# Kernel tuning notes

Measured on AMD Instinct MI355X. Metric: run time of the kernel, lower is better.

The kernel has to match this reference:

```python
import jax, jax.numpy as jnp
import numpy as np

NEG = -1e12


def setup_inputs() -> dict:
    key = jax.random.key(0)
    ks = jax.random.split(key, 6)
    B, S, D, H = 32, 2048, 1024, 1024  # batch, seq, dec/enc dim, hidden
    last_state = jax.random.normal(ks[0], (B, D), dtype=jnp.float32)
    enc_outputs = jax.random.normal(ks[1], (B, S, D), dtype=jnp.float32)
    attn_masks = jax.random.randint(ks[2], (B, S), 0, 2, dtype=jnp.int32)
    W = jax.random.normal(ks[3], (H, 2 * D), dtype=jnp.float32) * 0.02
    b = jax.random.normal(ks[4], (H,), dtype=jnp.float32) * 0.02
    V = jax.random.normal(ks[5], (H,), dtype=jnp.float32)
    return {"last_state": last_state, "enc_outputs": enc_outputs,
            "attn_masks": attn_masks, "W": W, "b": b, "V": V}


def reference(last_state, enc_outputs, attn_masks, W, b, V):
    # Split W to avoid materializing the [B,S,2D] concat:
    # concat([h, e]) @ W.T == h @ Wh.T + e @ We.T
    D = last_state.shape[-1]
    Wh, We = W[:, :D], W[:, D:]
    # hidden part: [B,H], broadcast over seq
    h_part = jnp.einsum('bd,hd->bh', last_state, Wh)  # [B,H]
    e_part = jnp.einsum('bsd,hd->bsh', enc_outputs, We)  # [B,S,H]
    sim = jnp.tanh(h_part[:, None, :] + e_part + b)  # [B,S,H]
    scores = jnp.einsum('bsh,h->bs', sim, V)  # [B,S]
    scores = jnp.where(attn_masks != 1, jnp.float32(NEG), scores)
    attn_weights = jax.nn.softmax(scores, axis=1)  # [B,S]
    context = jnp.einsum('bs,bsd->bd', attn_weights, enc_outputs)  # [B,D]
    return context, attn_weights, scores
```

## Files before the change

kernel.cpp:

```cpp
#include <hip/hip_runtime.h>
#include <math.h>
#include <stdint.h>

#define B_ 32
#define S_ 2048
#define D_ 1024
#define H_ 1024
#define NEGV -1000000000000.0f

typedef __attribute__((ext_vector_type(8))) short bf16x8;
typedef __attribute__((ext_vector_type(8))) _Float16 f16x8;
typedef __attribute__((ext_vector_type(4))) float f32x4;

static __device__ __forceinline__ unsigned short f2bf(float x) {
    union { float f; unsigned u; } v; v.f = x;
    unsigned r = v.u + 0x7FFF + ((v.u >> 16) & 1);
    return (unsigned short)(r >> 16);
}
static __device__ __forceinline__ float bf2f(unsigned short h) {
    union { float f; unsigned u; } v; v.u = ((unsigned)h) << 16; return v.f;
}
static __device__ __forceinline__ unsigned short f2h(float x) {
    _Float16 h = (_Float16)x; unsigned short u;
    __builtin_memcpy(&u, &h, 2); return u;
}
static __device__ __forceinline__ float h2f(unsigned short u) {
    _Float16 h; __builtin_memcpy(&h, &u, 2); return (float)h;
}
static __device__ __forceinline__ float tanh_fast(float x) {
    float e = __expf(2.f * x);
    return 1.f - 2.f / (e + 1.f);
}
static __device__ __forceinline__ void gl_lds16(unsigned short* lds, const unsigned short* g) {
    __builtin_amdgcn_global_load_lds(
        (const __attribute__((address_space(1))) unsigned int*)(const void*)g,
        (__attribute__((address_space(3))) unsigned int*)(void*)lds,
        16, 0, 0);
}

__global__ __launch_bounds__(256) void k_W_f16(const float* __restrict__ W,
                                               unsigned short* __restrict__ out) {
    int idx = blockIdx.x * 256 + threadIdx.x;
    int h = idx >> 7, kc = idx & 127;
    const float* src = W + (size_t)h * (2 * D_) + D_ + kc * 8;
    float4 a = *(const float4*)src;
    float4 c4 = *(const float4*)(src + 4);
    float v[8] = {a.x, a.y, a.z, a.w, c4.x, c4.y, c4.z, c4.w};
    unsigned short t[8];
#pragma unroll
    for (int j = 0; j < 8; ++j) t[j] = f2h(v[j]);
    uint4 w;
    w.x = t[0] | ((unsigned)t[1] << 16); w.y = t[2] | ((unsigned)t[3] << 16);
    w.z = t[4] | ((unsigned)t[5] << 16); w.w = t[6] | ((unsigned)t[7] << 16);
    int g = kc >> 4, cc = kc & 15;
    int dst = g * 128 + ((cc ^ (h & 15)) << 3);
    *(uint4*)(out + (size_t)h * D_ + dst) = w;
}

__global__ __launch_bounds__(256) void k_hpart(const float* __restrict__ ls,
                                               const float* __restrict__ W,
                                               float* __restrict__ hp) {
    int bh = blockIdx.x * 256 + threadIdx.x;
    int b = bh >> 10, h = bh & 1023;
    const float* lsr = ls + b * D_;
    const float* wr  = W + (size_t)h * (2 * D_);
    float acc = 0.f;
#pragma unroll 4
    for (int d = 0; d < D_; d += 4) {
        float4 a = *(const float4*)(lsr + d);
        float4 w = *(const float4*)(wr + d);
        acc += a.x * w.x + a.y * w.y + a.z * w.z + a.w * w.w;
    }
    hp[bh] = acc;
}

__global__ __launch_bounds__(512, 2) void k_scores_m128(
    const float* __restrict__ enc,
    const unsigned short* __restrict__ Wf16,
    const float* __restrict__ hp, const float* __restrict__ bias,
    const float* __restrict__ V, float* __restrict__ spart)
{
    extern __shared__ unsigned short smem[];
    unsigned short* smemA = smem;
    unsigned short* smemB = smem + 16384;

    const int tid  = threadIdx.x;
    const int lane = tid & 63, wid = tid >> 6;
    const int wm = wid >> 2, wn = wid & 3;
    const int l15 = lane & 15, lhi = lane >> 4;

    const int bid  = blockIdx.x;
    const int wgid = (bid & 7) * 256 + (bid >> 3);
    const int mt = wgid >> 2, nt = wgid & 3;
    const int m0 = mt * 128;
    const int nt256 = nt * 256;
    const int b = m0 >> 11;

    const size_t boff = (size_t)(nt256 + wid * 32 + (lane >> 4)) * D_ + (lane & 15) * 8;
    const int ldsb = wid * 4096;

    f32x4 acc[4][4];
#pragma unroll
    for (int i = 0; i < 4; ++i)
#pragma unroll
        for (int j = 0; j < 4; ++j)
            acc[i][j] = (f32x4){0.f, 0.f, 0.f, 0.f};

    const int swz = l15;

    float4 ar0[4], ar1[4];

#define LOAD_A(KOFS) do {                                                           \
    _Pragma("unroll")                                                               \
    for (int s_ = 0; s_ < 4; ++s_) {                                                \
        int p_ = tid + s_ * 512;                                                    \
        int row_ = p_ >> 4, pc_ = p_ & 15;                                          \
        const float* ap_ = enc + (size_t)(m0 + row_) * D_ + (KOFS) + pc_ * 8;       \
        ar0[s_] = *(const float4*)ap_;                                              \
        ar1[s_] = *(const float4*)(ap_ + 4);                                        \
    }                                                                               \
} while (0)
#define WRITE_A() do {                                                              \
    _Pragma("unroll")                                                               \
    for (int s_ = 0; s_ < 4; ++s_) {                                                \
        int p_ = tid + s_ * 512;                                                    \
        int row_ = p_ >> 4, pc_ = p_ & 15;                                          \
        float v_[8] = {ar0[s_].x, ar0[s_].y, ar0[s_].z, ar0[s_].w,                  \
                       ar1[s_].x, ar1[s_].y, ar1[s_].z, ar1[s_].w};                 \
        unsigned short t_[8];                                                       \
        _Pragma("unroll")                                                           \
        for (int j_ = 0; j_ < 8; ++j_) t_[j_] = f2h(v_[j_]);                        \
        uint4 w_;                                                                   \
        w_.x = t_[0] | ((unsigned)t_[1] << 16); w_.y = t_[2] | ((unsigned)t_[3] << 16); \
        w_.z = t_[4] | ((unsigned)t_[5] << 16); w_.w = t_[6] | ((unsigned)t_[7] << 16); \
        *(uint4*)&smemA[row_ * 128 + ((pc_ ^ (row_ & 15)) << 3)] = w_;              \
    }                                                                               \
} while (0)

#define STAGE_B(KOFS) do {                                                          \
    _Pragma("unroll")                                                               \
    for (int j_ = 0; j_ < 8; ++j_)                                                  \
        gl_lds16(&smemB[ldsb + j_ * 512], Wf16 + boff + (size_t)j_ * 4 * D_ + (KOFS)); \
} while (0)

#define LDA(AR, KS) do {                                                            \
    _Pragma("unroll")                                                               \
    for (int fi_ = 0; fi_ < 4; ++fi_) {                                             \
        int row_ = wm * 64 + fi_ * 16 + l15;                                        \
        int ch_  = ((KS) * 4 + lhi) ^ swz;                                          \
        AR[fi_] = *(const f16x8*)&smemA[row_ * 128 + ch_ * 8];                      \
    }                                                                               \
} while (0)
#define LDB(BR, KS) do {                                                            \
    _Pragma("unroll")                                                               \
    for (int fi_ = 0; fi_ < 4; ++fi_) {                                             \
        int row_ = wn * 64 + fi_ * 16 + l15;                                        \
        int ch_  = ((KS) * 4 + lhi) ^ swz;                                          \
        BR[fi_] = *(const f16x8*)&smemB[row_ * 128 + ch_ * 8];                      \
    }                                                                               \
} while (0)
#define MFMA16(AR, BR) do {                                                         \
    _Pragma("unroll")                                                               \
    for (int fi_ = 0; fi_ < 4; ++fi_)                                               \
    _Pragma("unroll")                                                               \
        for (int fj_ = 0; fj_ < 4; ++fj_)                                           \
            acc[fi_][fj_] = __builtin_amdgcn_mfma_f32_16x16x32_f16(                 \
                AR[fi_], BR[fj_], acc[fi_][fj_], 0, 0, 0);                          \
} while (0)

    LOAD_A(0);
    WRITE_A();
    STAGE_B(0);
    __syncthreads();

    f16x8 a[4], bk[4];
#pragma unroll 1
    for (int t = 0; t < 8; ++t) {
        const int kofs = (t + 1) * 128;

        if (t < 7) LOAD_A(kofs);

#pragma unroll
        for (int ks = 0; ks < 4; ++ks) {
            LDB(bk, ks);
            LDA(a, ks);
            MFMA16(a, bk);
        }

        __syncthreads();

        if (t < 7) {
            WRITE_A();
            STAGE_B(kofs);
        }

        __syncthreads();
    }

    float hb[4], vv[4];
#pragma unroll
    for (int fn = 0; fn < 4; ++fn) {
        int h = nt256 + wn * 64 + fn * 16 + l15;
        hb[fn] = hp[b * H_ + h] + bias[h];
        vv[fn] = V[h];
    }
    float* s_red = (float*)smem;
#pragma unroll
    for (int fm = 0; fm < 4; ++fm)
#pragma unroll
        for (int rg = 0; rg < 4; ++rg) {
            float rs = 0.f;
#pragma unroll
            for (int fn = 0; fn < 4; ++fn)
                rs += tanh_fast(acc[fm][fn][rg] + hb[fn]) * vv[fn];
            rs += __shfl_xor(rs, 1, 16);
            rs += __shfl_xor(rs, 2, 16);
            rs += __shfl_xor(rs, 4, 16);
            rs += __shfl_xor(rs, 8, 16);
            if (l15 == 0)
                s_red[wn * 128 + wm * 64 + fm * 16 + lhi * 4 + rg] = rs;
        }
    __syncthreads();
    if (tid < 128) {
        float v = s_red[tid] + s_red[128 + tid] + s_red[256 + tid] + s_red[384 + tid];
        spart[(size_t)nt * 65536 + m0 + tid] = v;
    }
#undef LOAD_A
#undef WRITE_A
#undef STAGE_B
#undef LDA
#undef LDB
#undef MFMA16
}

__global__ __launch_bounds__(256) void k_softmax_fold(const float* __restrict__ spart,
                                                      const int* __restrict__ mask,
                                                      float* __restrict__ scores_out,
                                                      float* __restrict__ weights) {
    __shared__ float red[8];
    int b = blockIdx.x, tid = threadIdx.x;
    float vals[8];
    float mx = -INFINITY;
#pragma unroll
    for (int i = 0; i < 8; ++i) {
        int m = b * S_ + tid + i * 256;
        float s = spart[m] + spart[65536 + m] + spart[131072 + m] + spart[196608 + m];
        s = (mask[m] == 1) ? s : NEGV;
        scores_out[m] = s;
        vals[i] = s;
        mx = fmaxf(mx, s);
    }
    for (int off = 32; off; off >>= 1) mx = fmaxf(mx, __shfl_xor(mx, off, 64));
    int wave = tid >> 6;
    if ((tid & 63) == 0) red[wave] = mx;
    __syncthreads();
    mx = fmaxf(fmaxf(red[0], red[1]), fmaxf(red[2], red[3]));
    float sum = 0.f;
#pragma unroll
    for (int i = 0; i < 8; ++i) {
        vals[i] = expf(vals[i] - mx);
        sum += vals[i];
    }
    for (int off = 32; off; off >>= 1) sum += __shfl_xor(sum, off, 64);
    if ((tid & 63) == 0) red[4 + wave] = sum;
    __syncthreads();
    sum = red[4] + red[5] + red[6] + red[7];
    float inv = 1.f / sum;
#pragma unroll
    for (int i = 0; i < 8; ++i)
        weights[b * S_ + tid + i * 256] = vals[i] * inv;
}

__global__ __launch_bounds__(256) void k_ctx_partial_f32(const float* __restrict__ weights,
                                                         const float* __restrict__ enc,
                                                         float* __restrict__ part) {
    int b = blockIdx.x >> 4;
    int chunk = blockIdx.x & 15;
    int tid = threadIdx.x;
    int d0 = tid * 4;
    float4 acc = {0.f, 0.f, 0.f, 0.f};
    int s0 = chunk * 128;
    const float* wrow = weights + b * S_;
    for (int s = s0; s < s0 + 128; ++s) {
        float w = wrow[s];
        if (w != 0.f) {
            float4 e = *(const float4*)(enc + (size_t)(b * S_ + s) * D_ + d0);
            acc.x += w * e.x; acc.y += w * e.y; acc.z += w * e.z; acc.w += w * e.w;
        }
    }
    *(float4*)(part + (size_t)blockIdx.x * D_ + d0) = acc;
}

__global__ __launch_bounds__(256) void k_ctx_reduce(const float* __restrict__ part,
                                                    float* __restrict__ ctx) {
    int bd = blockIdx.x * 256 + threadIdx.x;
    int b = bd >> 10, d = bd & 1023;
    float acc = 0.f;
#pragma unroll
    for (int c = 0; c < 16; ++c)
        acc += part[(size_t)(b * 16 + c) * D_ + d];
    ctx[bd] = acc;
}

__global__ __launch_bounds__(256) void k_splitW_lin(const float* __restrict__ W,
                                                    unsigned short* __restrict__ hi,
                                                    unsigned short* __restrict__ lo) {
    int idx = blockIdx.x * 256 + threadIdx.x;
    int h = idx >> 7, kc = idx & 127;
    const float* src = W + (size_t)h * (2 * D_) + D_ + kc * 8;
    float4 a = *(const float4*)src;
    float4 c = *(const float4*)(src + 4);
    float v[8] = {a.x, a.y, a.z, a.w, c.x, c.y, c.z, c.w};
    unsigned short th[8], tl[8];
#pragma unroll
    for (int j = 0; j < 8; ++j) {
        th[j] = f2bf(v[j]);
        tl[j] = f2bf(v[j] - bf2f(th[j]));
    }
    uint4 hw, lw;
    hw.x = th[0] | ((unsigned)th[1] << 16); hw.y = th[2] | ((unsigned)th[3] << 16);
    hw.z = th[4] | ((unsigned)th[5] << 16); hw.w = th[6] | ((unsigned)th[7] << 16);
    lw.x = tl[0] | ((unsigned)tl[1] << 16); lw.y = tl[2] | ((unsigned)tl[3] << 16);
    lw.z = tl[4] | ((unsigned)tl[5] << 16); lw.w = tl[6] | ((unsigned)tl[7] << 16);
    *(uint4*)(hi + (size_t)h * D_ + kc * 8) = hw;
    *(uint4*)(lo + (size_t)h * D_ + kc * 8) = lw;
}

__global__ __launch_bounds__(256, 2) void k_scores_mfma_fb(
    const float* __restrict__ enc,
    const unsigned short* __restrict__ Whi,
    const unsigned short* __restrict__ Wlo,
    const float* __restrict__ hp,
    const float* __restrict__ bias,
    const float* __restrict__ V,
    const int* __restrict__ mask,
    float* __restrict__ scores_out)
{
    __shared__ __align__(16) unsigned short smem[4 * 8192];
    unsigned short* sAhi = smem;
    unsigned short* sAlo = smem + 8192;
    unsigned short* sBhi = smem + 16384;
    unsigned short* sBlo = smem + 24576;

    const int tid  = threadIdx.x;
    const int lane = tid & 63, wid = tid >> 6;
    const int wr = wid >> 1, wc = wid & 1;
    const int l15 = lane & 15, lhi = lane >> 4;
    const int m0 = blockIdx.x * 128;
    const int b  = m0 >> 11;

    float rowsum[4][4] = {};
    float4 pa[8];
    uint4  pbh[4], pbl[4];

#define STAGE_LOAD(NB, KB) do {                                            \
    _Pragma("unroll")                                                      \
    for (int i_ = 0; i_ < 4; ++i_) {                                       \
        int c_ = tid + i_ * 256;                                           \
        int r_ = c_ >> 3, kc_ = c_ & 7;                                    \
        const float* ap_ = enc + (size_t)(m0 + r_) * D_ + (KB) * 64 + kc_ * 8; \
        pa[2 * i_]     = *(const float4*)ap_;                              \
        pa[2 * i_ + 1] = *(const float4*)(ap_ + 4);                        \
        size_t bo_ = (size_t)((NB) * 128 + r_) * D_ + (KB) * 64 + kc_ * 8; \
        pbh[i_] = *(const uint4*)(Whi + bo_);                              \
        pbl[i_] = *(const uint4*)(Wlo + bo_);                              \
    }                                                                      \
} while (0)

#define STAGE_WRITE() do {                                                 \
    _Pragma("unroll")                                                      \
    for (int i_ = 0; i_ < 4; ++i_) {                                       \
        int c_ = tid + i_ * 256;                                           \
        int sc_ = c_ ^ ((c_ >> 3) & 7);                                    \
        float vv_[8] = {pa[2*i_].x, pa[2*i_].y, pa[2*i_].z, pa[2*i_].w,    \
                        pa[2*i_+1].x, pa[2*i_+1].y, pa[2*i_+1].z, pa[2*i_+1].w}; \
        unsigned short th_[8], tl_[8];                                     \
        _Pragma("unroll")                                                  \
        for (int j_ = 0; j_ < 8; ++j_) {                                   \
            th_[j_] = f2bf(vv_[j_]);                                       \
            tl_[j_] = f2bf(vv_[j_] - bf2f(th_[j_]));                       \
        }                                                                  \
        uint4 hw_, lw_;                                                    \
        hw_.x = th_[0] | ((unsigned)th_[1] << 16); hw_.y = th_[2] | ((unsigned)th_[3] << 16); \
        hw_.z = th_[4] | ((unsigned)th_[5] << 16); hw_.w = th_[6] | ((unsigned)th_[7] << 16); \
        lw_.x = tl_[0] | ((unsigned)tl_[1] << 16); lw_.y = tl_[2] | ((unsigned)tl_[3] << 16); \
        lw_.z = tl_[4] | ((unsigned)tl_[5] << 16); lw_.w = tl_[6] | ((unsigned)tl_[7] << 16); \
        *(uint4*)&sAhi[sc_ * 8] = hw_;                                     \
        *(uint4*)&sAlo[sc_ * 8] = lw_;                                     \
        *(uint4*)&sBhi[sc_ * 8] = pbh[i_];                                 \
        *(uint4*)&sBlo[sc_ * 8] = pbl[i_];                                 \
    }                                                                      \
} while (0)

    STAGE_LOAD(0, 0);

    for (int nb = 0; nb < 8; ++nb) {
        f32x4 acc[4][4];
#pragma unroll
        for (int i = 0; i < 4; ++i)
#pragma unroll
            for (int j = 0; j < 4; ++j)
                acc[i][j] = (f32x4){0.f, 0.f, 0.f, 0.f};

        for (int kb = 0; kb < 16; ++kb) {
            __syncthreads();
            STAGE_WRITE();
            __syncthreads();
            int nkb = kb + 1, nnb = nb;
            if (nkb == 16) { nkb = 0; nnb = nb + 1; }
            if (nnb < 8) STAGE_LOAD(nnb, nkb);

#pragma unroll
            for (int ks = 0; ks < 2; ++ks) {
                bf16x8 bh[4], bl[4];
#pragma unroll
                for (int fn = 0; fn < 4; ++fn) {
                    int rB = wc * 64 + fn * 16 + l15;
                    int ch = (rB * 8 + ks * 4 + lhi) ^ (rB & 7);
                    bh[fn] = *(const bf16x8*)&sBhi[ch * 8];
                    bl[fn] = *(const bf16x8*)&sBlo[ch * 8];
                }
#pragma unroll
                for (int fm = 0; fm < 4; ++fm) {
                    int rA = wr * 64 + fm * 16 + l15;
                    int ch = (rA * 8 + ks * 4 + lhi) ^ (rA & 7);
                    bf16x8 ah = *(const bf16x8*)&sAhi[ch * 8];
                    bf16x8 al = *(const bf16x8*)&sAlo[ch * 8];
#pragma unroll
                    for (int fn = 0; fn < 4; ++fn) {
                        acc[fm][fn] = __builtin_amdgcn_mfma_f32_16x16x32_bf16(ah, bh[fn], acc[fm][fn], 0, 0, 0);
                        acc[fm][fn] = __builtin_amdgcn_mfma_f32_16x16x32_bf16(ah, bl[fn], acc[fm][fn], 0, 0, 0);
                        acc[fm][fn] = __builtin_amdgcn_mfma_f32_16x16x32_bf16(al, bh[fn], acc[fm][fn], 0, 0, 0);
                    }
                }
            }
        }

        int n0 = nb * 128;
#pragma unroll
        for (int fn = 0; fn < 4; ++fn) {
            int n = n0 + wc * 64 + fn * 16 + l15;
            float hbv = hp[b * H_ + n] + bias[n];
            float vvv = V[n];
#pragma unroll
            for (int fm = 0; fm < 4; ++fm) {
                f32x4 a = acc[fm][fn];
#pragma unroll
                for (int rg = 0; rg < 4; ++rg)
                    rowsum[fm][rg] += tanh_fast(a[rg] + hbv) * vvv;
            }
        }
    }

    __syncthreads();
    float* s_red = (float*)smem;
#pragma unroll
    for (int fm = 0; fm < 4; ++fm)
#pragma unroll
        for (int rg = 0; rg < 4; ++rg) {
            float v = rowsum[fm][rg];
            v += __shfl_xor(v, 1, 16);
            v += __shfl_xor(v, 2, 16);
            v += __shfl_xor(v, 4, 16);
            v += __shfl_xor(v, 8, 16);
            if (l15 == 0)
                s_red[wc * 128 + wr * 64 + fm * 16 + lhi * 4 + rg] = v;
        }
    __syncthreads();
    if (tid < 128) {
        int m = m0 + tid;
        float sc = s_red[tid] + s_red[128 + tid];
        scores_out[m] = (mask[m] == 1) ? sc : NEGV;
    }
#undef STAGE_LOAD
#undef STAGE_WRITE
}

__global__ __launch_bounds__(256) void k_softmax(const float* __restrict__ scores,
                                                 float* __restrict__ weights) {
    __shared__ float red[8];
    int b = blockIdx.x;
    int tid = threadIdx.x;
    const float* srow = scores + b * S_;
    float vals[8];
    float mx = -INFINITY;
#pragma unroll
    for (int i = 0; i < 8; ++i) {
        vals[i] = srow[tid + i * 256];
        mx = fmaxf(mx, vals[i]);
    }
    for (int off = 32; off; off >>= 1) mx = fmaxf(mx, __shfl_xor(mx, off, 64));
    int wave = tid >> 6;
    if ((tid & 63) == 0) red[wave] = mx;
    __syncthreads();
    mx = fmaxf(fmaxf(red[0], red[1]), fmaxf(red[2], red[3]));
    float sum = 0.f;
#pragma unroll
    for (int i = 0; i < 8; ++i) {
        vals[i] = expf(vals[i] - mx);
        sum += vals[i];
    }
    for (int off = 32; off; off >>= 1) sum += __shfl_xor(sum, off, 64);
    if ((tid & 63) == 0) red[4 + wave] = sum;
    __syncthreads();
    sum = red[4] + red[5] + red[6] + red[7];
    float inv = 1.f / sum;
#pragma unroll
    for (int i = 0; i < 8; ++i)
        weights[b * S_ + tid + i * 256] = vals[i] * inv;
}

extern "C" void kernel_launch(void* const* d_in, const int* in_sizes, int n_in,
                              void* d_out, int out_size, void* d_ws, size_t ws_size,
                              hipStream_t stream) {
    const float* ls   = (const float*)d_in[0];
    const float* enc  = (const float*)d_in[1];
    const int*   mask = (const int*)d_in[2];
    const float* W    = (const float*)d_in[3];
    const float* bias = (const float*)d_in[4];
    const float* V    = (const float*)d_in[5];

    float* out     = (float*)d_out;
    float* ctx     = out;
    float* weights = out + 32768;
    float* scores  = out + 98304;

    const size_t need = 2097152ull + 131072ull + 1048576ull + 2097152ull;

    if (ws_size >= need) {
        unsigned short* Wf16 = (unsigned short*)d_ws;
        float* hp    = (float*)(Wf16 + 1048576);
        float* spart = hp + 32768;
        float* part  = spart + 262144;

        hipFuncSetAttribute((const void*)k_scores_m128,
                            hipFuncAttributeMaxDynamicSharedMemorySize, 98304);

        k_W_f16<<<512, 256, 0, stream>>>(W, Wf16);
        k_hpart<<<128, 256, 0, stream>>>(ls, W, hp);
        k_scores_m128<<<2048, 512, 98304, stream>>>(enc, Wf16, hp, bias, V, spart);
        k_softmax_fold<<<32, 256, 0, stream>>>(spart, mask, scores, weights);
        k_ctx_partial_f32<<<512, 256, 0, stream>>>(weights, enc, part);
        k_ctx_reduce<<<128, 256, 0, stream>>>(part, ctx);
    } else {
        unsigned short* Whi = (unsigned short*)d_ws;
        unsigned short* Wlo = Whi + 1048576;
        float* hp   = (float*)(Wlo + 1048576);
        float* part = hp + 32768;

        k_splitW_lin<<<512, 256, 0, stream>>>(W, Whi, Wlo);
        k_hpart<<<128, 256, 0, stream>>>(ls, W, hp);
        k_scores_mfma_fb<<<512, 256, 0, stream>>>(enc, Whi, Wlo, hp, bias, V, mask, scores);
        k_softmax<<<32, 256, 0, stream>>>(scores, weights);
        k_ctx_partial_f32<<<512, 256, 0, stream>>>(weights, enc, part);
        k_ctx_reduce<<<128, 256, 0, stream>>>(part, ctx);
    }
}
```

Baseline: 288.1 us.

## Halve K-tile and drop register prefetch to raise scores GEMM occupancy

The scores GEMM kernel now uses a K-tile of 64 instead of 128, halving LDS per block to 48KB, and raises launch bounds to 4 blocks per CU. The register-staged software prefetch of the A tile is removed: each iteration loads and converts A and stages B, syncs, then computes. The W fp16 layout and swizzle are changed to match the 64-wide tile. Latency hiding now depends on more resident waves instead of explicit overlap, at the cost of twice as many barriers per K sweep and a tighter register budget.

```diff
diff --git a/kernel.cpp b/kernel.cpp
--- a/kernel.cpp
+++ b/kernel.cpp
@@ -52,8 +52,8 @@
     uint4 w;
     w.x = t[0] | ((unsigned)t[1] << 16); w.y = t[2] | ((unsigned)t[3] << 16);
     w.z = t[4] | ((unsigned)t[5] << 16); w.w = t[6] | ((unsigned)t[7] << 16);
-    int g = kc >> 4, cc = kc & 15;
-    int dst = g * 128 + ((cc ^ (h & 15)) << 3);
+    int g = kc >> 3, cc = kc & 7;
+    int dst = g * 64 + ((cc ^ (h & 7)) << 3);
     *(uint4*)(out + (size_t)h * D_ + dst) = w;
 }
 
@@ -74,7 +74,7 @@
     hp[bh] = acc;
 }
 
-__global__ __launch_bounds__(512, 2) void k_scores_m128(
+__global__ __launch_bounds__(512, 4) void k_scores_occ(
     const float* __restrict__ enc,
     const unsigned short* __restrict__ Wf16,
     const float* __restrict__ hp, const float* __restrict__ bias,
@@ -82,7 +82,7 @@
 {
     extern __shared__ unsigned short smem[];
     unsigned short* smemA = smem;
-    unsigned short* smemB = smem + 16384;
+    unsigned short* smemB = smem + 8192;
 
     const int tid  = threadIdx.x;
     const int lane = tid & 63, wid = tid >> 6;
@@ -96,8 +96,8 @@
     const int nt256 = nt * 256;
     const int b = m0 >> 11;
 
-    const size_t boff = (size_t)(nt256 + wid * 32 + (lane >> 4)) * D_ + (lane & 15) * 8;
-    const int ldsb = wid * 4096;
+    const size_t boff = (size_t)(nt256 + wid * 16 + (lane >> 3)) * D_ + (lane & 7) * 8;
+    const int ldsb = wid * 1024;
 
     f32x4 acc[4][4];
 #pragma unroll
@@ -106,41 +106,36 @@
         for (int j = 0; j < 4; ++j)
             acc[i][j] = (f32x4){0.f, 0.f, 0.f, 0.f};
 
-    const int swz = l15;
-
-    float4 ar0[4], ar1[4];
-
-#define LOAD_A(KOFS) do {                                                           \
+    const int swz = l15 & 7;
+
+#define STAGE_A(KOFS) do {                                                          \
     _Pragma("unroll")                                                               \
-    for (int s_ = 0; s_ < 4; ++s_) {                                                \
+    for (int s_ = 0; s_ < 2; ++s_) {                                                \
         int p_ = tid + s_ * 512;                                                    \
-        int row_ = p_ >> 4, pc_ = p_ & 15;                                          \
+        int row_ = p_ >> 3, pc_ = p_ & 7;                                           \
         const float* ap_ = enc + (size_t)(m0 + row_) * D_ + (KOFS) + pc_ * 8;       \
-        ar0[s_] = *(const float4*)ap_;                                              \
-        ar1[s_] = *(const float4*)(ap_ + 4);                                        \
-    }                                                                               \
-} while (0)
-#define WRITE_A() do {                                                              \
-    _Pragma("unroll")                                                               \
-    for (int s_ = 0; s_ < 4; ++s_) {                                                \
-        int p_ = tid + s_ * 512;                                                    \
-        int row_ = p_ >> 4, pc_ = p_ & 15;                                          \
-        float v_[8] = {ar0[s_].x, ar0[s_].y, ar0[s_].z, ar0[s_].w,                  \
-                       ar1[s_].x, ar1[s_].y, ar1[s_].z, ar1[s_].w};                 \
+        float4 x0_ = *(const float4*)ap_;                                           \
+        float4 x1_ = *(const float4*)(ap_ + 4);                                     \
+        float v_[8] = {x0_.x, x0_.y, x0_.z, x0_.w, x1_.x, x1_.y, x1_.z, x1_.w};     \
         unsigned short t_[8];                                                       \
         _Pragma("unroll")                                                           \
         for (int j_ = 0; j_ < 8; ++j_) t_[j_] = f2h(v_[j_]);                        \
         uint4 w_;                                                                   \
         w_.x = t_[0] | ((unsigned)t_[1] << 16); w_.y = t_[2] | ((unsigned)t_[3] << 16); \
         w_.z = t_[4] | ((unsigned)t_[5] << 16); w_.w = t_[6] | ((unsigned)t_[7] << 16); \
-        *(uint4*)&smemA[row_ * 128 + ((pc_ ^ (row_ & 15)) << 3)] = w_;              \
+        *(uint4*)&smemA[row_ * 64 + ((pc_ ^ (row_ & 7)) << 3)] = w_;                \
     }                                                                               \
 } while (0)
 
 #define STAGE_B(KOFS) do {                                                          \
-    _Pragma("unroll")                                                               \
-    for (int j_ = 0; j_ < 8; ++j_)                                                  \
-        gl_lds16(&smemB[ldsb + j_ * 512], Wf16 + boff + (size_t)j_ * 4 * D_ + (KOFS)); \
+    unsigned short* d0_ = &smemB[ldsb];                                             \
+    unsigned short* d1_ = &smemB[8192 + ldsb];                                      \
+    const unsigned short* s0_ = Wf16 + boff + (KOFS);                               \
+    const unsigned short* s1_ = Wf16 + boff + 131072 + (KOFS);                      \
+    gl_lds16(d0_, s0_);                                                             \
+    gl_lds16(d0_ + 512, s0_ + 8192);                                                \
+    gl_lds16(d1_, s1_);                                                             \
+    gl_lds16(d1_ + 512, s1_ + 8192);                                                \
 } while (0)
 
 #define LDA(AR, KS) do {                                                            \
@@ -148,7 +143,7 @@
     for (int fi_ = 0; fi_ < 4; ++fi_) {                                             \
         int row_ = wm * 64 + fi_ * 16 + l15;                                        \
         int ch_  = ((KS) * 4 + lhi) ^ swz;                                          \
-        AR[fi_] = *(const f16x8*)&smemA[row_ * 128 + ch_ * 8];                      \
+        AR[fi_] = *(const f16x8*)&smemA[row_ * 64 + ch_ * 8];                       \
     }                                                                               \
 } while (0)
 #define LDB(BR, KS) do {                                                            \
@@ -156,7 +151,7 @@
     for (int fi_ = 0; fi_ < 4; ++fi_) {                                             \
         int row_ = wn * 64 + fi_ * 16 + l15;                                        \
         int ch_  = ((KS) * 4 + lhi) ^ swz;                                          \
-        BR[fi_] = *(const f16x8*)&smemB[row_ * 128 + ch_ * 8];                      \
+        BR[fi_] = *(const f16x8*)&smemB[row_ * 64 + ch_ * 8];                       \
     }                                                                               \
 } while (0)
 #define MFMA16(AR, BR) do {                                                         \
@@ -168,30 +163,20 @@
                 AR[fi_], BR[fj_], acc[fi_][fj_], 0, 0, 0);                          \
 } while (0)
 
-    LOAD_A(0);
-    WRITE_A();
-    STAGE_B(0);
-    __syncthreads();
-
     f16x8 a[4], bk[4];
 #pragma unroll 1
-    for (int t = 0; t < 8; ++t) {
-        const int kofs = (t + 1) * 128;
-
-        if (t < 7) LOAD_A(kofs);
-
-#pragma unroll
-        for (int ks = 0; ks < 4; ++ks) {
+    for (int t = 0; t < 16; ++t) {
+        const int kofs = t * 64;
+
+        STAGE_B(kofs);
+        STAGE_A(kofs);
+        __syncthreads();
+
+#pragma unroll
+        for (int ks = 0; ks < 2; ++ks) {
             LDB(bk, ks);
             LDA(a, ks);
             MFMA16(a, bk);
-        }
-
-        __syncthreads();
-
-        if (t < 7) {
-            WRITE_A();
-            STAGE_B(kofs);
         }
 
         __syncthreads();
@@ -225,8 +210,7 @@
         float v = s_red[tid] + s_red[128 + tid] + s_red[256 + tid] + s_red[384 + tid];
         spart[(size_t)nt * 65536 + m0 + tid] = v;
     }
-#undef LOAD_A
-#undef WRITE_A
+#undef STAGE_A
 #undef STAGE_B
 #undef LDA
 #undef LDB
@@ -533,12 +517,12 @@
         float* spart = hp + 32768;
         float* part  = spart + 262144;
 
-        hipFuncSetAttribute((const void*)k_scores_m128,
-                            hipFuncAttributeMaxDynamicSharedMemorySize, 98304);
+        hipFuncSetAttribute((const void*)k_scores_occ,
+                            hipFuncAttributeMaxDynamicSharedMemorySize, 49152);
 
         k_W_f16<<<512, 256, 0, stream>>>(W, Wf16);
         k_hpart<<<128, 256, 0, stream>>>(ls, W, hp);
-        k_scores_m128<<<2048, 512, 98304, stream>>>(enc, Wf16, hp, bias, V, spart);
+        k_scores_occ<<<2048, 512, 49152, stream>>>(enc, Wf16, hp, bias, V, spart);
         k_softmax_fold<<<32, 256, 0, stream>>>(spart, mask, scores, weights);
         k_ctx_partial_f32<<<512, 256, 0, stream>>>(weights, enc, part);
         k_ctx_reduce<<<128, 256, 0, stream>>>(part, ctx);
```

Result: faster. 253.2 us (-12.1%).
